# Kernel tuning notes

Hardware: AMD Instinct MI355X
Metric: run time of the kernel (lower is better)

The kernel has to match this reference:

```python
import jax, jax.numpy as jnp
import numpy as np

IN_FEATURES = 4096
OUT_FEATURES = 1024
BATCH = 16384
WERR = 1.0
BERR = 1.0


def setup_inputs() -> dict:
    key = jax.random.key(0)
    kx, kw = jax.random.split(key)
    X = jax.random.normal(kx, (BATCH, IN_FEATURES), dtype=jnp.float32)
    # glorot_uniform init for W, zeros for bias (as in Keras layer)
    limit = np.sqrt(6.0 / (IN_FEATURES + OUT_FEATURES)).astype(np.float32)
    W = jax.random.uniform(kw, (IN_FEATURES, OUT_FEATURES), dtype=jnp.float32,
                           minval=-limit, maxval=limit)
    bias = jnp.zeros((1, OUT_FEATURES), dtype=jnp.float32)
    return {"X": X, "W": W, "bias": bias}


def reference(X, W, bias):
    # Binarize weights/bias with sign(), scaled by Werr/Berr, then dense matmul.
    Wb = jnp.sign(W) * WERR          # [in, out], values in {-1, 0, +1}
    bb = jnp.sign(bias) * BERR       # [1, out]
    Z = jnp.matmul(X, Wb) + bb       # [batch, out]
    return Z
```

## Files before the change

### kernel.cpp

```cpp
#include <hip/hip_runtime.h>

#define M_DIM 16384
#define N_DIM 1024
#define K_DIM 4096

#define BM 256
#define BN 256
#define BK 64
#define NT (K_DIM / BK)

typedef __attribute__((ext_vector_type(4))) float f32x4;
typedef __attribute__((ext_vector_type(8))) short bf16x8;
typedef __attribute__((ext_vector_type(8))) unsigned short u16x8;

static __device__ __forceinline__ short f2bf(float f) {
  union { __bf16 h; short s; } u;
  u.h = (__bf16)f;
  return u.s;
}

static __device__ __forceinline__ void load_lds16(const void* g, void* l) {
  __builtin_amdgcn_global_load_lds(
      (const __attribute__((address_space(1))) void*)g,
      (__attribute__((address_space(3))) void*)l, 16, 0, 0);
}

__global__ __launch_bounds__(256) void wsign_transpose(
    const float* __restrict__ W, unsigned short* __restrict__ WbT) {
  __shared__ unsigned short tile[64][72];
  const int t  = (int)threadIdx.x;
  const int k0 = (int)(blockIdx.x >> 4) * 64;
  const int n0 = (int)(blockIdx.x & 15) * 64;
#pragma unroll
  for (int p = 0; p < 4; ++p) {
    const int r = p * 16 + (t >> 4);
    const int c = (t & 15) * 4;
    const float* src = W + (size_t)(k0 + r) * N_DIM + n0 + c;
#pragma unroll
    for (int j = 0; j < 4; ++j) {
      const float w = src[j];
      tile[r][c + j] = (w > 0.f) ? (unsigned short)0x3F80u
                                 : ((w < 0.f) ? (unsigned short)0xBF80u
                                              : (unsigned short)0u);
    }
  }
  __syncthreads();
  const int n  = t >> 2;
  const int kg = (t & 3) * 16;
  u16x8 o0, o1;
#pragma unroll
  for (int j = 0; j < 8; ++j) o0[j] = tile[kg + j][n];
#pragma unroll
  for (int j = 0; j < 8; ++j) o1[j] = tile[kg + 8 + j][n];
  unsigned short* dst = WbT + (size_t)(n0 + n) * K_DIM + k0 + kg;
  *(u16x8*)dst       = o0;
  *(u16x8*)(dst + 8) = o1;
}

__global__ __launch_bounds__(512, 2) void gemm_bin(
    const float* __restrict__ X, const unsigned short* __restrict__ WbT,
    const float* __restrict__ bias, float* __restrict__ Z) {
  __shared__ __align__(16) unsigned short As[2][BM * BK];
  __shared__ __align__(16) unsigned short Bs[2][BN * BK];

  const int t   = (int)threadIdx.x;
  const int l   = t & 63;
  const int wid = t >> 6;
  const int wm  = wid >> 2;
  const int wn  = wid & 3;

  const int bid = (int)blockIdx.x;
  const int swz = (bid & 7) * 32 + (bid >> 3);
  const int m0  = (swz >> 2) * BM;
  const int n0  = (swz & 3) * BN;

  const int abase = (wm * 128 + (l & 15)) * BK;
  const int bbase = (wn * 64 + (l & 15)) * BK;
  const int axk0  = (((l >> 4) + 0) ^ (l & 7)) << 3;
  const int axk1  = (((l >> 4) + 4) ^ (l & 7)) << 3;

  const float* a_src[4];
  int a_dst[4];
#pragma unroll
  for (int i = 0; i < 4; ++i) {
    const int d = i * 512 + t;
    const int row = d >> 3, g = d & 7;
    a_src[i] = X + (size_t)(m0 + row) * K_DIM + g * 8;
    a_dst[i] = row * BK + ((g ^ (row & 7)) << 3);
  }
  const unsigned short* b_src[4];
  int b_dst[4];
#pragma unroll
  for (int i = 0; i < 4; ++i) {
    const int c = i * 512 + t;
    const int n = c >> 3, gp = c & 7;
    b_src[i] = WbT + (size_t)(n0 + n) * K_DIM + (gp ^ (n & 7)) * 8;
    b_dst[i] = c * 8;
  }

  f32x4 acc[8][4] = {};
  f32x4 areg[4][2];

#define STAGE_A_LOAD(KT)                                                  \
  {                                                                       \
    _Pragma("unroll") for (int i = 0; i < 4; ++i) {                       \
      areg[i][0] = *(const f32x4*)(a_src[i] + (KT));                      \
      areg[i][1] = *(const f32x4*)(a_src[i] + (KT) + 4);                  \
    }                                                                     \
  }
#define STAGE_A_WRITE(BUF)                                                \
  {                                                                       \
    _Pragma("unroll") for (int i = 0; i < 4; ++i) {                       \
      u16x8 v;                                                            \
      _Pragma("unroll") for (int j = 0; j < 4; ++j) {                     \
        v[j]     = (unsigned short)f2bf(areg[i][0][j]);                   \
        v[4 + j] = (unsigned short)f2bf(areg[i][1][j]);                   \
      }                                                                   \
      *(u16x8*)(&As[BUF][a_dst[i]]) = v;                                  \
    }                                                                     \
  }
#define STAGE_B(KT, BUF)                                                  \
  {                                                                       \
    _Pragma("unroll") for (int i = 0; i < 4; ++i)                         \
      load_lds16(b_src[i] + (KT), &Bs[BUF][b_dst[i]]);                    \
  }
#define COMPUTE(CUR)                                                      \
  {                                                                       \
    const unsigned short* Ab = As[CUR];                                   \
    const unsigned short* Bb = Bs[CUR];                                   \
    _Pragma("unroll") for (int kk = 0; kk < 2; ++kk) {                    \
      const int axk = kk ? axk1 : axk0;                                   \
      bf16x8 bf[4];                                                       \
      _Pragma("unroll") for (int ni = 0; ni < 4; ++ni)                    \
        bf[ni] = *(const bf16x8*)(Bb + bbase + ni * 1024 + axk);          \
      _Pragma("unroll") for (int mi = 0; mi < 8; ++mi) {                  \
        const bf16x8 af = *(const bf16x8*)(Ab + abase + mi * 1024 + axk); \
        _Pragma("unroll") for (int ni = 0; ni < 4; ++ni)                  \
          acc[mi][ni] = __builtin_amdgcn_mfma_f32_16x16x32_bf16(          \
              af, bf[ni], acc[mi][ni], 0, 0, 0);                          \
      }                                                                   \
    }                                                                     \
  }

  STAGE_A_LOAD(0);
  STAGE_B(0, 0);
  STAGE_A_WRITE(0);
  __syncthreads();

  int cur = 0;
  for (int tt = 0; tt < NT - 1; ++tt) {
    const int ktn = (tt + 1) * BK;
    STAGE_A_LOAD(ktn);
    STAGE_B(ktn, cur ^ 1);
    COMPUTE(cur);
    STAGE_A_WRITE(cur ^ 1);
    __syncthreads();
    cur ^= 1;
  }
  COMPUTE(cur);

#pragma unroll
  for (int ni = 0; ni < 4; ++ni) {
    const int col = n0 + wn * 64 + ni * 16 + (l & 15);
    const float b  = bias[col];
    const float bs = (b > 0.f) ? 1.f : ((b < 0.f) ? -1.f : 0.f);
#pragma unroll
    for (int mi = 0; mi < 8; ++mi) {
      const int row = m0 + wm * 128 + mi * 16 + ((l >> 4) << 2);
#pragma unroll
      for (int j = 0; j < 4; ++j)
        Z[(size_t)(row + j) * N_DIM + col] = acc[mi][ni][j] + bs;
    }
  }
#undef STAGE_A_LOAD
#undef STAGE_A_WRITE
#undef STAGE_B
#undef COMPUTE
}

__global__ __launch_bounds__(256) void naive_fb(
    const float* __restrict__ X, const float* __restrict__ W,
    const float* __restrict__ bias, float* __restrict__ Z) {
  const size_t id = (size_t)blockIdx.x * 256 + threadIdx.x;
  const int m = (int)(id >> 10), n = (int)(id & 1023);
  float acc = 0.f;
  for (int k = 0; k < K_DIM; ++k) {
    const float w = W[(size_t)k * N_DIM + n];
    const float s = (w > 0.f) ? 1.f : ((w < 0.f) ? -1.f : 0.f);
    acc += X[(size_t)m * K_DIM + k] * s;
  }
  const float b = bias[n];
  Z[id] = acc + ((b > 0.f) ? 1.f : ((b < 0.f) ? -1.f : 0.f));
}

extern "C" void kernel_launch(void* const* d_in, const int* in_sizes, int n_in,
                              void* d_out, int out_size, void* d_ws, size_t ws_size,
                              hipStream_t stream) {
  const float* X    = (const float*)d_in[0];
  const float* W    = (const float*)d_in[1];
  const float* bias = (const float*)d_in[2];
  float* Z = (float*)d_out;

  const size_t need = (size_t)N_DIM * K_DIM * sizeof(unsigned short);
  if (ws_size >= need) {
    unsigned short* WbT = (unsigned short*)d_ws;
    wsign_transpose<<<dim3((K_DIM / 64) * (N_DIM / 64)), dim3(256), 0, stream>>>(W, WbT);
    gemm_bin<<<dim3((M_DIM / BM) * (N_DIM / BN)), dim3(512), 0, stream>>>(X, WbT, bias, Z);
  } else {
    naive_fb<<<dim3((size_t)M_DIM * N_DIM / 256), dim3(256), 0, stream>>>(X, W, bias, Z);
  }
}
```

Baseline: 192.0 us.

## Shrink GEMM tiles to 128x128x32 with 256 threads for higher occupancy

```diff
diff --git a/kernel.cpp b/kernel.cpp
--- a/kernel.cpp
+++ b/kernel.cpp
@@ -4,9 +4,9 @@
 #define N_DIM 1024
 #define K_DIM 4096
 
-#define BM 256
-#define BN 256
-#define BK 64
+#define BM 128
+#define BN 128
+#define BK 32
 #define NT (K_DIM / BK)
 
 typedef __attribute__((ext_vector_type(4))) float f32x4;
@@ -57,7 +57,7 @@
   *(u16x8*)(dst + 8) = o1;
 }
 
-__global__ __launch_bounds__(512, 2) void gemm_bin(
+__global__ __launch_bounds__(256, 3) void gemm_occ(
     const float* __restrict__ X, const unsigned short* __restrict__ WbT,
     const float* __restrict__ bias, float* __restrict__ Z) {
   __shared__ __align__(16) unsigned short As[2][BM * BK];
@@ -66,80 +66,78 @@
   const int t   = (int)threadIdx.x;
   const int l   = t & 63;
   const int wid = t >> 6;
-  const int wm  = wid >> 2;
-  const int wn  = wid & 3;
+  const int wm  = wid >> 1;
+  const int wn  = wid & 1;
 
   const int bid = (int)blockIdx.x;
-  const int swz = (bid & 7) * 32 + (bid >> 3);
-  const int m0  = (swz >> 2) * BM;
-  const int n0  = (swz & 3) * BN;
-
-  const int abase = (wm * 128 + (l & 15)) * BK;
+  const int swz = (bid & 7) * 128 + (bid >> 3);
+  const int m0  = (swz >> 3) * BM;
+  const int n0  = (swz & 7) * BN;
+
+  const int axx   = ((((l >> 4) ^ (l & 3) ^ ((l >> 2) & 3)) & 3)) << 3;
+  const int abase = (wm * 64 + (l & 15)) * BK;
   const int bbase = (wn * 64 + (l & 15)) * BK;
-  const int axk0  = (((l >> 4) + 0) ^ (l & 7)) << 3;
-  const int axk1  = (((l >> 4) + 4) ^ (l & 7)) << 3;
-
-  const float* a_src[4];
-  int a_dst[4];
-#pragma unroll
-  for (int i = 0; i < 4; ++i) {
-    const int d = i * 512 + t;
-    const int row = d >> 3, g = d & 7;
-    a_src[i] = X + (size_t)(m0 + row) * K_DIM + g * 8;
-    a_dst[i] = row * BK + ((g ^ (row & 7)) << 3);
-  }
-  const unsigned short* b_src[4];
-  int b_dst[4];
-#pragma unroll
-  for (int i = 0; i < 4; ++i) {
-    const int c = i * 512 + t;
-    const int n = c >> 3, gp = c & 7;
-    b_src[i] = WbT + (size_t)(n0 + n) * K_DIM + (gp ^ (n & 7)) * 8;
-    b_dst[i] = c * 8;
-  }
-
-  f32x4 acc[8][4] = {};
-  f32x4 areg[4][2];
+
+  const int rA = t >> 1, hA = t & 1;
+  const float* srcA = X + (size_t)(m0 + rA) * K_DIM + hA * 16;
+  const int fr   = (rA & 3) ^ ((rA >> 2) & 3);
+  const int g0   = (2 * hA) ^ fr;
+  const int adst0 = rA * BK + ((g0 & 3) << 3);
+  const int adst1 = rA * BK + (((g0 ^ 1) & 3) << 3);
+
+  const unsigned short* bsrc[2];
+  int bdst[2];
+#pragma unroll
+  for (int i = 0; i < 2; ++i) {
+    const int c = i * 256 + t;
+    const int n = c >> 2, p = c & 3;
+    const int q = p ^ ((n & 3) ^ ((n >> 2) & 3));
+    bsrc[i] = WbT + (size_t)(n0 + n) * K_DIM + q * 8;
+    bdst[i] = c * 8;
+  }
+
+  f32x4 acc[4][4] = {};
+  f32x4 areg[4];
 
 #define STAGE_A_LOAD(KT)                                                  \
   {                                                                       \
-    _Pragma("unroll") for (int i = 0; i < 4; ++i) {                       \
-      areg[i][0] = *(const f32x4*)(a_src[i] + (KT));                      \
-      areg[i][1] = *(const f32x4*)(a_src[i] + (KT) + 4);                  \
+    areg[0] = *(const f32x4*)(srcA + (KT));                               \
+    areg[1] = *(const f32x4*)(srcA + (KT) + 4);                           \
+    areg[2] = *(const f32x4*)(srcA + (KT) + 8);                           \
+    areg[3] = *(const f32x4*)(srcA + (KT) + 12);                          \
+  }
+#define STAGE_A_WRITE(BUF)                                                \
+  {                                                                       \
+    u16x8 v0, v1;                                                         \
+    _Pragma("unroll") for (int q = 0; q < 4; ++q) {                       \
+      v0[q]     = (unsigned short)f2bf(areg[0][q]);                       \
+      v0[4 + q] = (unsigned short)f2bf(areg[1][q]);                       \
+      v1[q]     = (unsigned short)f2bf(areg[2][q]);                       \
+      v1[4 + q] = (unsigned short)f2bf(areg[3][q]);                       \
     }                                                                     \
-  }
-#define STAGE_A_WRITE(BUF)                                                \
-  {                                                                       \
-    _Pragma("unroll") for (int i = 0; i < 4; ++i) {                       \
-      u16x8 v;                                                            \
-      _Pragma("unroll") for (int j = 0; j < 4; ++j) {                     \
-        v[j]     = (unsigned short)f2bf(areg[i][0][j]);                   \
-        v[4 + j] = (unsigned short)f2bf(areg[i][1][j]);                   \
-      }                                                                   \
-      *(u16x8*)(&As[BUF][a_dst[i]]) = v;                                  \
+    *(u16x8*)(&As[BUF][adst0]) = v0;                                      \
+    *(u16x8*)(&As[BUF][adst1]) = v1;                                      \
+  }
+#define STAGE_B(KT, BUF)                                                  \
+  {                                                                       \
+    load_lds16(bsrc[0] + (KT), &Bs[BUF][bdst[0]]);                        \
+    load_lds16(bsrc[1] + (KT), &Bs[BUF][bdst[1]]);                        \
+  }
+#define COMPUTE(CUR)                                                      \
+  {                                                                       \
+    const unsigned short* Ab = &As[CUR][0];                               \
+    const unsigned short* Bb = &Bs[CUR][0];                               \
+    bf16x8 bf[4];                                                         \
+    _Pragma("unroll") for (int nj = 0; nj < 4; ++nj)                      \
+      bf[nj] = *(const bf16x8*)(Bb + bbase + nj * 512 + axx);             \
+    __builtin_amdgcn_s_setprio(1);                                        \
+    _Pragma("unroll") for (int mi = 0; mi < 4; ++mi) {                    \
+      const bf16x8 af = *(const bf16x8*)(Ab + abase + mi * 512 + axx);    \
+      _Pragma("unroll") for (int nj = 0; nj < 4; ++nj)                    \
+        acc[mi][nj] = __builtin_amdgcn_mfma_f32_16x16x32_bf16(            \
+            af, bf[nj], acc[mi][nj], 0, 0, 0);                            \
     }                                                                     \
-  }
-#define STAGE_B(KT, BUF)                                                  \
-  {                                                                       \
-    _Pragma("unroll") for (int i = 0; i < 4; ++i)                         \
-      load_lds16(b_src[i] + (KT), &Bs[BUF][b_dst[i]]);                    \
-  }
-#define COMPUTE(CUR)                                                      \
-  {                                                                       \
-    const unsigned short* Ab = As[CUR];                                   \
-    const unsigned short* Bb = Bs[CUR];                                   \
-    _Pragma("unroll") for (int kk = 0; kk < 2; ++kk) {                    \
-      const int axk = kk ? axk1 : axk0;                                   \
-      bf16x8 bf[4];                                                       \
-      _Pragma("unroll") for (int ni = 0; ni < 4; ++ni)                    \
-        bf[ni] = *(const bf16x8*)(Bb + bbase + ni * 1024 + axk);          \
-      _Pragma("unroll") for (int mi = 0; mi < 8; ++mi) {                  \
-        const bf16x8 af = *(const bf16x8*)(Ab + abase + mi * 1024 + axk); \
-        _Pragma("unroll") for (int ni = 0; ni < 4; ++ni)                  \
-          acc[mi][ni] = __builtin_amdgcn_mfma_f32_16x16x32_bf16(          \
-              af, bf[ni], acc[mi][ni], 0, 0, 0);                          \
-      }                                                                   \
-    }                                                                     \
+    __builtin_amdgcn_s_setprio(0);                                        \
   }
 
   STAGE_A_LOAD(0);
@@ -147,29 +145,28 @@
   STAGE_A_WRITE(0);
   __syncthreads();
 
-  int cur = 0;
   for (int tt = 0; tt < NT - 1; ++tt) {
+    const int cur = tt & 1;
     const int ktn = (tt + 1) * BK;
     STAGE_A_LOAD(ktn);
     STAGE_B(ktn, cur ^ 1);
     COMPUTE(cur);
     STAGE_A_WRITE(cur ^ 1);
     __syncthreads();
-    cur ^= 1;
-  }
-  COMPUTE(cur);
-
-#pragma unroll
-  for (int ni = 0; ni < 4; ++ni) {
-    const int col = n0 + wn * 64 + ni * 16 + (l & 15);
+  }
+  COMPUTE((NT - 1) & 1);
+
+#pragma unroll
+  for (int nj = 0; nj < 4; ++nj) {
+    const int col = n0 + wn * 64 + nj * 16 + (l & 15);
     const float b  = bias[col];
     const float bs = (b > 0.f) ? 1.f : ((b < 0.f) ? -1.f : 0.f);
 #pragma unroll
-    for (int mi = 0; mi < 8; ++mi) {
-      const int row = m0 + wm * 128 + mi * 16 + ((l >> 4) << 2);
+    for (int mi = 0; mi < 4; ++mi) {
+      const int row = m0 + wm * 64 + mi * 16 + ((l >> 4) << 2);
 #pragma unroll
       for (int j = 0; j < 4; ++j)
-        Z[(size_t)(row + j) * N_DIM + col] = acc[mi][ni][j] + bs;
+        Z[(size_t)(row + j) * N_DIM + col] = acc[mi][nj][j] + bs;
     }
   }
 #undef STAGE_A_LOAD
@@ -201,11 +198,11 @@
   const float* bias = (const float*)d_in[2];
   float* Z = (float*)d_out;
 
-  const size_t need = (size_t)N_DIM * K_DIM * sizeof(unsigned short);
-  if (ws_size >= need) {
+  const size_t needW = (size_t)N_DIM * K_DIM * sizeof(unsigned short);
+  if (ws_size >= needW) {
     unsigned short* WbT = (unsigned short*)d_ws;
     wsign_transpose<<<dim3((K_DIM / 64) * (N_DIM / 64)), dim3(256), 0, stream>>>(W, WbT);
-    gemm_bin<<<dim3((M_DIM / BM) * (N_DIM / BN)), dim3(512), 0, stream>>>(X, WbT, bias, Z);
+    gemm_occ<<<dim3((M_DIM / BM) * (N_DIM / BN)), dim3(256), 0, stream>>>(X, WbT, bias, Z);
   } else {
     naive_fb<<<dim3((size_t)M_DIM * N_DIM / 256), dim3(256), 0, stream>>>(X, W, bias, Z);
   }
```

Result: slower. 285.2 us (+48.6%).
